# Optimization experiments

Hardware: AMD Instinct MI355X
Metric: run time of the kernel (lower is better)

The kernel has to match this reference:

```python
import jax, jax.numpy as jnp
import numpy as np

B, F_, E = 4096, 40, 64
T, M, H = 2, 3, 1
EPS = 1e-5


def setup_inputs() -> dict:
    key = jax.random.key(0)
    ks = jax.random.split(key, 8)
    def xavier(k, shape, fan_in, fan_out):
        a = float(np.sqrt(6.0 / (fan_in + fan_out)))
        return jax.random.uniform(k, shape, jnp.float32, -a, a)
    x = jax.random.normal(ks[0], (B, F_, E), jnp.float32)
    masker = xavier(ks[1], (T, M, F_, F_), F_, F_)
    ln_gamma = jnp.ones((F_,), jnp.float32)
    ln_beta = jnp.zeros((F_,), jnp.float32)
    w_t = xavier(ks[2], (1, T, H, 2 * E, E), 2 * E, E)
    b_t = xavier(ks[3], (T, H, F_, E), F_, E)
    nbn = T * F_ * 2 * E
    bn_gamma = jnp.ones((nbn,), jnp.float32)
    bn_beta = jnp.zeros((nbn,), jnp.float32)
    bn_mean = jnp.zeros((nbn,), jnp.float32)
    bn_var = jnp.ones((nbn,), jnp.float32)
    gate_w = xavier(ks[4], (F_ * E, F_), F_ * E, F_)
    gate_b = jnp.zeros((F_,), jnp.float32)
    return {"x": x, "masker": masker, "ln_gamma": ln_gamma, "ln_beta": ln_beta,
            "w_t": w_t, "b_t": b_t, "bn_gamma": bn_gamma, "bn_beta": bn_beta,
            "bn_mean": bn_mean, "bn_var": bn_var, "gate_w": gate_w, "gate_b": gate_b}


def reference(x, masker, ln_gamma, ln_beta, w_t, b_t, bn_gamma, bn_beta, bn_mean, bn_var, gate_w, gate_b):
    b = x.shape[0]
    # broadcast input across towers: (B, T, F, E)
    xt = jnp.broadcast_to(x[:, None], (b, T, F_, E))
    # masked adjacency construction (per tower)
    adj = jax.nn.relu(jnp.prod(masker, axis=1))            # (T, F, F)
    mask = (adj != 0).astype(x.dtype)
    # LayerNorm over dim -2 (applied to transposed adj in torch)
    t = jnp.swapaxes(adj, -1, -2)
    mu = t.mean(-1, keepdims=True)
    var = t.var(-1, keepdims=True)
    t = (t - mu) / jnp.sqrt(var + EPS) * ln_gamma + ln_beta
    adj = jnp.swapaxes(t, -1, -2)
    logits = adj + (1.0 - mask) * (-1e9) + jnp.eye(F_, dtype=x.dtype)
    adj = jax.nn.softmax(logits, axis=1) * mask            # softmax over source-field dim
    xcur = xt
    for idx in range(H):
        # neighbor aggregation: nei[b,t,f,e] = sum_g x[b,t,g,e] * adj[t,g,f]
        nei = jnp.einsum('btge,tgf->btfe', xcur, adj)
        xc = jnp.concatenate([xcur, nei], axis=-1)         # (B, T, F, 2E)
        flat = xc.reshape(b, -1)                           # BatchNorm1d, inference mode
        flat = (flat - bn_mean) / jnp.sqrt(bn_var + EPS) * bn_gamma + bn_beta
        xc = flat.reshape(b, T, F_, 2 * E)
        xcur = jnp.einsum('btfk,tke->btfe', xc, w_t[0, :, idx]) + b_t[:, idx]
    # gating over fields
    g = xcur.reshape(b, T, F_ * E) @ gate_w + gate_b       # (B, T, F)
    w = jax.nn.softmax(g, axis=2)
    return jnp.sum(xcur * w[..., None], axis=2)            # (B, T, E)
```

## Files before the change

### kernel.cpp

```cpp
#include <hip/hip_runtime.h>
#include <hip/hip_bf16.h>
#include <math.h>

#define Fdim 40
#define Edim 64
#define Tdim 2
#define EPSV 1e-5f

typedef __attribute__((ext_vector_type(8))) short short8;
typedef __attribute__((ext_vector_type(4))) float f32x4;

__device__ __forceinline__ short f2b(float f) {
    unsigned u = __builtin_bit_cast(unsigned, f);
    unsigned r = (u + 0x7fffu + ((u >> 16) & 1u)) >> 16;
    return (short)r;
}
__device__ __forceinline__ float b2f(short h) {
    unsigned u = ((unsigned)(unsigned short)h) << 16;
    return __builtin_bit_cast(float, u);
}
__device__ __forceinline__ f32x4 mfma16(short8 a, short8 b, f32x4 c) {
    return __builtin_amdgcn_mfma_f32_16x16x32_bf16(a, b, c, 0, 0, 0);
}
__device__ __forceinline__ int swz(int f, int e2 ) {
    return (f * 128 + e2) ^ ((f & 7) << 4);
}

#define BUFS 5152


__global__ void adj_kernel(const float* __restrict__ masker,
                           const float* __restrict__ ln_gamma,
                           const float* __restrict__ ln_beta,
                           short* __restrict__ adjF) {
    const int t = blockIdx.x;
    const int tid = threadIdx.x;
    __shared__ float araw[Fdim][Fdim];

    for (int i = tid; i < Fdim * Fdim; i += 64) {
        int g = i / Fdim, ff = i % Fdim;
        const float* mb = masker + t * (3 * Fdim * Fdim) + g * Fdim + ff;
        float p = mb[0] * mb[Fdim * Fdim] * mb[2 * Fdim * Fdim];
        araw[g][ff] = p > 0.f ? p : 0.f;
    }
    __syncthreads();

    const int f = tid;
    float vals[Fdim];
    if (f < 40) {
        float mu = 0.f, m2 = 0.f;
        #pragma unroll
        for (int g = 0; g < Fdim; ++g) {
            float v = araw[g][f];
            mu += v; m2 += v * v;
        }
        mu *= (1.f / Fdim); m2 *= (1.f / Fdim);
        float inv = rsqrtf(m2 - mu * mu + EPSV);

        float mx = -1e30f;
        #pragma unroll
        for (int g = 0; g < Fdim; ++g) {
            float v = araw[g][f];
            float l = (v - mu) * inv * ln_gamma[g] + ln_beta[g];
            if (v == 0.f) l += -1e9f;
            if (g == f) l += 1.f;
            vals[g] = l;
            mx = fmaxf(mx, l);
        }
        float den = 0.f;
        #pragma unroll
        for (int g = 0; g < Fdim; ++g) {
            float p = expf(vals[g] - mx);
            vals[g] = p;
            den += p;
        }
        float rden = 1.f / den;
        #pragma unroll
        for (int g = 0; g < Fdim; ++g) {
            float msk = (araw[g][f] != 0.f) ? 1.f : 0.f;
            vals[g] = vals[g] * rden * msk;
        }
    }
    if (f < 48) {
        int er = f & 15, mt = f >> 4;
        short8* dst = (short8*)adjF;
        #pragma unroll
        for (int kt = 0; kt < 2; ++kt) {
            #pragma unroll
            for (int qq = 0; qq < 4; ++qq) {
                short8 v;
                #pragma unroll
                for (int j = 0; j < 8; ++j) {
                    int g = kt * 32 + qq * 8 + j;
                    v[j] = (f < 40 && g < 40) ? f2b(vals[g]) : (short)0;
                }
                dst[((t * 3 + mt) * 2 + kt) * 64 + qq * 16 + er] = v;
            }
        }
    }
}

__global__ void prep_kernel(const float* __restrict__ w_t,
                            const float* __restrict__ gate_w,
                            const float* __restrict__ bn_gamma,
                            const float* __restrict__ bn_beta,
                            const float* __restrict__ bn_mean,
                            const float* __restrict__ bn_var,
                            const float* __restrict__ b_t,
                            short* __restrict__ WF,
                            short* __restrict__ gwF,
                            float* __restrict__ bnSxF,
                            float* __restrict__ bnOxF,
                            float* __restrict__ bn2SF,
                            float* __restrict__ bn2OF,
                            float* __restrict__ btF) {
    int i = blockIdx.x * 256 + threadIdx.x;
    if (i < 16384) {
        int j = i & 7, l = (i >> 3) & 63, nt = (i >> 9) & 3, kt = (i >> 11) & 3, t = i >> 13;
        int k = kt * 32 + (l >> 4) * 8 + j, e = nt * 16 + (l & 15);
        WF[i] = f2b(w_t[t * 8192 + k * 64 + e]);
    } else if (i < 139264) {
        int idx = i - 16384;
        int j = idx & 7, l = (idx >> 3) & 63, r = idx >> 9;
        int nt = r % 3, kk = r / 3;
        int fo = nt * 16 + (l & 15), k = kk * 32 + (l >> 4) * 8 + j;
        gwF[idx] = (fo < 40) ? f2b(gate_w[(size_t)k * 40 + fo]) : (short)0;
    } else if (i < 145408) {
        int idx = i - 139264;
        int c = idx & 3, l = (idx >> 2) & 63, h = (idx >> 8) & 1, kt = (idx >> 9) & 1, tm = idx >> 10;
        int mt = tm % 3, t = tm / 3;
        int f = mt * 16 + (l & 15), k = kt * 32 + (l >> 4) * 8 + h * 4 + c;
        float sv = 0.f, ov = 0.f;
        if (f < 40) {
            int src = t * 5120 + f * 128 + k;
            sv = bn_gamma[src] * rsqrtf(bn_var[src] + EPSV);
            ov = bn_beta[src] - bn_mean[src] * sv;
        }
        bnSxF[idx] = sv; bnOxF[idx] = ov;
    } else if (i < 151552) {
        int idx = i - 145408;
        int rr = idx & 3, l = (idx >> 2) & 63, nt = (idx >> 8) & 3, tm = idx >> 10;
        int mt = tm % 3, t = tm / 3;
        int f = mt * 16 + (l >> 4) * 4 + rr, e = nt * 16 + (l & 15);
        float sv = 0.f, ov = 0.f;
        if (f < 40) {
            int src = t * 5120 + f * 128 + 64 + e;
            sv = bn_gamma[src] * rsqrtf(bn_var[src] + EPSV);
            ov = bn_beta[src] - bn_mean[src] * sv;
        }
        bn2SF[idx] = sv; bn2OF[idx] = ov;
    } else if (i < 157696) {
        int idx = i - 151552;
        int rr = idx & 3, l = (idx >> 2) & 63, nt = (idx >> 8) & 3, tm = idx >> 10;
        int mt = tm % 3, t = tm / 3;
        int f = mt * 16 + (l >> 4) * 4 + rr, e = nt * 16 + (l & 15);
        btF[idx] = (f < 40) ? b_t[t * 2560 + f * 64 + e] : 0.f;
    }
}

__global__ __launch_bounds__(512, 4) void main_kernel(
    const float* __restrict__ x,
    const short* __restrict__ adjF,
    const short* __restrict__ WF,
    const short* __restrict__ gwF,
    const f32x4* __restrict__ bnSxF,
    const f32x4* __restrict__ bnOxF,
    const f32x4* __restrict__ bn2SF,
    const f32x4* __restrict__ bn2OF,
    const f32x4* __restrict__ btF,
    const float* __restrict__ gate_b,
    float* __restrict__ out)
{
    extern __shared__ char smem[];
    const int tid = threadIdx.x;
    const int w = tid >> 6, lane = tid & 63;
    const int er = lane & 15, q = lane >> 4;
    const int s = w >> 1, t = w & 1;
    const int bbase = blockIdx.x * 4;

    char* buf = smem + w * BUFS;
    f32x4* gred = (f32x4*)(smem + 8 * BUFS);
    float* g_lds = (float*)(smem + 8 * BUFS + 6144);

    const float* xb = x + (size_t)(bbase + s) * 2560;
    const short8* adjF8 = (const short8*)adjF;
    const short8* WF8   = (const short8*)WF;
    const short8* gwF8  = (const short8*)gwF;

    short8 Bf[2][4];
    #pragma unroll
    for (int nt = 0; nt < 4; ++nt) {
        const float* xe = xb + nt * 16 + er;
        short8 v0;
        #pragma unroll
        for (int j = 0; j < 8; ++j) v0[j] = f2b(xe[(q * 8 + j) * 64]);
        Bf[0][nt] = v0;
        short8 v1 = {0, 0, 0, 0, 0, 0, 0, 0};
        if (q == 0) {
            #pragma unroll
            for (int j = 0; j < 8; ++j) v1[j] = f2b(xe[(32 + j) * 64]);
        }
        Bf[1][nt] = v1;
    }

    #pragma unroll
    for (int mt = 0; mt < 3; ++mt) {
        short8 A0 = adjF8[((t * 3 + mt) * 2 + 0) * 64 + lane];
        short8 A1 = adjF8[((t * 3 + mt) * 2 + 1) * 64 + lane];
        #pragma unroll
        for (int nt = 0; nt < 4; ++nt) {
            f32x4 z = {0.f, 0.f, 0.f, 0.f};
            z = mfma16(A0, Bf[0][nt], z);
            f32x4 acc = mfma16(A1, Bf[1][nt], z);
            f32x4 s2 = bn2SF[((t * 3 + mt) * 4 + nt) * 64 + lane];
            f32x4 o2 = bn2OF[((t * 3 + mt) * 4 + nt) * 64 + lane];
            int e = nt * 16 + er;
            #pragma unroll
            for (int r = 0; r < 4; ++r) {
                int f = mt * 16 + q * 4 + r;
                if (f < 40) {
                    float vv = acc[r] * s2[r] + o2[r];
                    *(short*)(buf + swz(f, e * 2)) = f2b(vv);
                }
            }
        }
    }

    #pragma unroll
    for (int mt = 0; mt < 3; ++mt) {
        f32x4 acc[4];
        #pragma unroll
        for (int nt = 0; nt < 4; ++nt) { f32x4 z = {0.f,0.f,0.f,0.f}; acc[nt] = z; }
        #pragma unroll
        for (int kt = 0; kt < 4; ++kt) {
            short8 A;
            if (kt < 2) {
                int f = mt * 16 + er;
                if (f < 40) {
                    const float4* xp = (const float4*)(xb + f * 64 + kt * 32 + q * 8);
                    float4 x0 = xp[0], x1 = xp[1];
                    int fb = (((t * 3 + mt) * 2 + kt) * 2) * 64 + lane;
                    f32x4 s0 = bnSxF[fb], s1 = bnSxF[fb + 64];
                    f32x4 o0 = bnOxF[fb], o1 = bnOxF[fb + 64];
                    A[0] = f2b(x0.x * s0[0] + o0[0]);
                    A[1] = f2b(x0.y * s0[1] + o0[1]);
                    A[2] = f2b(x0.z * s0[2] + o0[2]);
                    A[3] = f2b(x0.w * s0[3] + o0[3]);
                    A[4] = f2b(x1.x * s1[0] + o1[0]);
                    A[5] = f2b(x1.y * s1[1] + o1[1]);
                    A[6] = f2b(x1.z * s1[2] + o1[2]);
                    A[7] = f2b(x1.w * s1[3] + o1[3]);
                } else {
                    short8 za = {0,0,0,0,0,0,0,0};
                    A = za;
                }
            } else {
                int f = mt * 16 + er;
                int fr = (f < 40) ? f : (f - 8);
                A = *(const short8*)(buf + swz(fr, (kt - 2) * 64 + q * 16));
            }
            #pragma unroll
            for (int nt = 0; nt < 4; ++nt) {
                short8 B = WF8[((t * 4 + kt) * 4 + nt) * 64 + lane];
                acc[nt] = mfma16(A, B, acc[nt]);
            }
        }
        #pragma unroll
        for (int nt = 0; nt < 4; ++nt) {
            f32x4 bt4 = btF[((t * 3 + mt) * 4 + nt) * 64 + lane];
            int e = nt * 16 + er;
            #pragma unroll
            for (int r = 0; r < 4; ++r) {
                int f = mt * 16 + q * 4 + r;
                if (f < 40) {
                    float vv = acc[nt][r] + bt4[r];
                    *(short*)(buf + swz(f, e * 2)) = f2b(vv);
                }
            }
        }
    }

    __syncthreads();

    f32x4 g0 = {0.f,0.f,0.f,0.f}, g1 = g0, g2 = g0;
    {
        const char* abase = smem + (er & 7) * BUFS;
        #pragma unroll
        for (int kk = 0; kk < 10; ++kk) {
            int step = w * 10 + kk;
            int k0 = step * 32;
            int f = k0 >> 6;
            short8 A = *(const short8*)(abase + swz(f, (k0 & 63) * 2 + q * 16));
            const short8* gp = gwF8 + (size_t)step * 3 * 64 + lane;
            g0 = mfma16(A, gp[0], g0);
            g1 = mfma16(A, gp[64], g1);
            g2 = mfma16(A, gp[128], g2);
        }
    }
    if (w < 4 && q < 2) {
        gred[(w * 3 + 0) * 32 + (lane & 31)] = g0;
        gred[(w * 3 + 1) * 32 + (lane & 31)] = g1;
        gred[(w * 3 + 2) * 32 + (lane & 31)] = g2;
    }
    __syncthreads();
    if (w >= 4 && q < 2) {
        gred[((w - 4) * 3 + 0) * 32 + (lane & 31)] += g0;
        gred[((w - 4) * 3 + 1) * 32 + (lane & 31)] += g1;
        gred[((w - 4) * 3 + 2) * 32 + (lane & 31)] += g2;
    }
    __syncthreads();

    if (tid < 192) {
        int nt = tid >> 6, l = tid & 63;
        if (l < 32) {
            int rer = l & 15, rq = l >> 4;
            f32x4 v = gred[(0 * 3 + nt) * 32 + l];
            #pragma unroll
            for (int ww = 1; ww < 4; ++ww) v += gred[(ww * 3 + nt) * 32 + l];
            int fo = nt * 16 + rer;
            if (fo < 40) {
                float gb = gate_b[fo];
                #pragma unroll
                for (int r = 0; r < 4; ++r)
                    g_lds[(rq * 4 + r) * 40 + fo] = v[r] + gb;
            }
        }
    }
    __syncthreads();

    {
        int st = tid >> 6, e = tid & 63;
        const float* gr = g_lds + st * 40;
        const char* bufr = smem + st * BUFS;
        float m = gr[0];
        #pragma unroll
        for (int f2 = 1; f2 < 40; ++f2) m = fmaxf(m, gr[f2]);
        float den = 0.f, o = 0.f;
        #pragma unroll
        for (int f2 = 0; f2 < 40; ++f2) {
            float p = __expf(gr[f2] - m);
            den += p;
            short xv = *(const short*)(bufr + swz(f2, e * 2));
            o += p * b2f(xv);
        }
        out[(size_t)(bbase * 2 + st) * 64 + e] = o / den;
    }
}

extern "C" void kernel_launch(void* const* d_in, const int* in_sizes, int n_in,
                              void* d_out, int out_size, void* d_ws, size_t ws_size,
                              hipStream_t stream) {
    (void)in_sizes; (void)n_in; (void)out_size; (void)ws_size;
    const float* x        = (const float*)d_in[0];
    const float* masker   = (const float*)d_in[1];
    const float* ln_gamma = (const float*)d_in[2];
    const float* ln_beta  = (const float*)d_in[3];
    const float* w_t      = (const float*)d_in[4];
    const float* b_t      = (const float*)d_in[5];
    const float* bn_gamma = (const float*)d_in[6];
    const float* bn_beta  = (const float*)d_in[7];
    const float* bn_mean  = (const float*)d_in[8];
    const float* bn_var   = (const float*)d_in[9];
    const float* gate_w   = (const float*)d_in[10];
    const float* gate_b   = (const float*)d_in[11];
    float* out = (float*)d_out;

    short* adjFp  = (short*)d_ws;
    short* WFp    = adjFp + 6144;
    short* gwFp   = WFp + 16384;
    float* bnSxFp = (float*)(gwFp + 122880);
    float* bnOxFp = bnSxFp + 6144;
    float* bn2SFp = bnOxFp + 6144;
    float* bn2OFp = bn2SFp + 6144;
    float* btFp   = bn2OFp + 6144;

    adj_kernel<<<Tdim, 64, 0, stream>>>(masker, ln_gamma, ln_beta, adjFp);
    prep_kernel<<<616, 256, 0, stream>>>(w_t, gate_w, bn_gamma, bn_beta, bn_mean,
                                         bn_var, b_t, WFp, gwFp, bnSxFp, bnOxFp,
                                         bn2SFp, bn2OFp, btFp);

    constexpr int SMEM_BYTES = 8 * BUFS + 4 * 3 * 32 * 16 + 8 * 40 * 4;
    main_kernel<<<1024, 512, SMEM_BYTES, stream>>>(
        x, adjFp, (const short*)WFp, (const short*)gwFp,
        (const f32x4*)bnSxFp, (const f32x4*)bnOxFp,
        (const f32x4*)bn2SFp, (const f32x4*)bn2OFp,
        (const f32x4*)btFp, gate_b, out);
}
```

Before: 73.76 us.

## Split main kernel into xcur and gate kernels via workspace, merge setup kernels

Merges the adjacency and weight-prep kernels into one launch to save a kernel launch. Splits the fused main kernel into an xcur kernel (256 threads, one wave per sample-tower) that writes bf16 intermediate results to a global workspace, and a gate kernel that reloads them and performs the gating GEMM and softmax. The aim is smaller blocks with better occupancy and less LDS per block. The cost is an extra global round trip of about 40MB of bf16 data plus one more launch, and the new path only runs when the workspace is large enough; otherwise it falls back to the original fused kernel.

```diff
diff --git a/kernel.cpp b/kernel.cpp
--- a/kernel.cpp
+++ b/kernel.cpp
@@ -29,92 +29,94 @@
 #define BUFS 5152
 
 
-__global__ void adj_kernel(const float* __restrict__ masker,
-                           const float* __restrict__ ln_gamma,
-                           const float* __restrict__ ln_beta,
-                           short* __restrict__ adjF) {
-    const int t = blockIdx.x;
+__global__ void setup_kernel(const float* __restrict__ masker,
+                             const float* __restrict__ ln_gamma,
+                             const float* __restrict__ ln_beta,
+                             const float* __restrict__ w_t,
+                             const float* __restrict__ gate_w,
+                             const float* __restrict__ bn_gamma,
+                             const float* __restrict__ bn_beta,
+                             const float* __restrict__ bn_mean,
+                             const float* __restrict__ bn_var,
+                             const float* __restrict__ b_t,
+                             short* __restrict__ adjF,
+                             short* __restrict__ WF,
+                             short* __restrict__ gwF,
+                             float* __restrict__ bnSxF,
+                             float* __restrict__ bnOxF,
+                             float* __restrict__ bn2SF,
+                             float* __restrict__ bn2OF,
+                             float* __restrict__ btF) {
+    const int bid = blockIdx.x;
     const int tid = threadIdx.x;
-    __shared__ float araw[Fdim][Fdim];
-
-    for (int i = tid; i < Fdim * Fdim; i += 64) {
-        int g = i / Fdim, ff = i % Fdim;
-        const float* mb = masker + t * (3 * Fdim * Fdim) + g * Fdim + ff;
-        float p = mb[0] * mb[Fdim * Fdim] * mb[2 * Fdim * Fdim];
-        araw[g][ff] = p > 0.f ? p : 0.f;
-    }
-    __syncthreads();
-
-    const int f = tid;
-    float vals[Fdim];
-    if (f < 40) {
-        float mu = 0.f, m2 = 0.f;
-        #pragma unroll
-        for (int g = 0; g < Fdim; ++g) {
-            float v = araw[g][f];
-            mu += v; m2 += v * v;
-        }
-        mu *= (1.f / Fdim); m2 *= (1.f / Fdim);
-        float inv = rsqrtf(m2 - mu * mu + EPSV);
-
-        float mx = -1e30f;
-        #pragma unroll
-        for (int g = 0; g < Fdim; ++g) {
-            float v = araw[g][f];
-            float l = (v - mu) * inv * ln_gamma[g] + ln_beta[g];
-            if (v == 0.f) l += -1e9f;
-            if (g == f) l += 1.f;
-            vals[g] = l;
-            mx = fmaxf(mx, l);
-        }
-        float den = 0.f;
-        #pragma unroll
-        for (int g = 0; g < Fdim; ++g) {
-            float p = expf(vals[g] - mx);
-            vals[g] = p;
-            den += p;
-        }
-        float rden = 1.f / den;
-        #pragma unroll
-        for (int g = 0; g < Fdim; ++g) {
-            float msk = (araw[g][f] != 0.f) ? 1.f : 0.f;
-            vals[g] = vals[g] * rden * msk;
-        }
-    }
-    if (f < 48) {
-        int er = f & 15, mt = f >> 4;
-        short8* dst = (short8*)adjF;
-        #pragma unroll
-        for (int kt = 0; kt < 2; ++kt) {
-            #pragma unroll
-            for (int qq = 0; qq < 4; ++qq) {
-                short8 v;
+
+    if (bid >= 616) {
+        const int t = bid - 616;
+        __shared__ float araw[Fdim][Fdim];
+        for (int i = tid; i < Fdim * Fdim; i += 256) {
+            int g = i / Fdim, ff = i % Fdim;
+            const float* mb = masker + t * (3 * Fdim * Fdim) + g * Fdim + ff;
+            float p = mb[0] * mb[Fdim * Fdim] * mb[2 * Fdim * Fdim];
+            araw[g][ff] = p > 0.f ? p : 0.f;
+        }
+        __syncthreads();
+
+        const int f = tid;
+        float vals[Fdim];
+        if (f < 40) {
+            float mu = 0.f, m2 = 0.f;
+            #pragma unroll
+            for (int g = 0; g < Fdim; ++g) {
+                float v = araw[g][f];
+                mu += v; m2 += v * v;
+            }
+            mu *= (1.f / Fdim); m2 *= (1.f / Fdim);
+            float inv = rsqrtf(m2 - mu * mu + EPSV);
+            float mx = -1e30f;
+            #pragma unroll
+            for (int g = 0; g < Fdim; ++g) {
+                float v = araw[g][f];
+                float l = (v - mu) * inv * ln_gamma[g] + ln_beta[g];
+                if (v == 0.f) l += -1e9f;
+                if (g == f) l += 1.f;
+                vals[g] = l;
+                mx = fmaxf(mx, l);
+            }
+            float den = 0.f;
+            #pragma unroll
+            for (int g = 0; g < Fdim; ++g) {
+                float p = expf(vals[g] - mx);
+                vals[g] = p;
+                den += p;
+            }
+            float rden = 1.f / den;
+            #pragma unroll
+            for (int g = 0; g < Fdim; ++g) {
+                float msk = (araw[g][f] != 0.f) ? 1.f : 0.f;
+                vals[g] = vals[g] * rden * msk;
+            }
+        }
+        if (f < 48) {
+            int er = f & 15, mt = f >> 4;
+            short8* dst = (short8*)adjF;
+            #pragma unroll
+            for (int kt = 0; kt < 2; ++kt) {
                 #pragma unroll
-                for (int j = 0; j < 8; ++j) {
-                    int g = kt * 32 + qq * 8 + j;
-                    v[j] = (f < 40 && g < 40) ? f2b(vals[g]) : (short)0;
+                for (int qq = 0; qq < 4; ++qq) {
+                    short8 v;
+                    #pragma unroll
+                    for (int j = 0; j < 8; ++j) {
+                        int g = kt * 32 + qq * 8 + j;
+                        v[j] = (f < 40 && g < 40) ? f2b(vals[g]) : (short)0;
+                    }
+                    dst[((t * 3 + mt) * 2 + kt) * 64 + qq * 16 + er] = v;
                 }
-                dst[((t * 3 + mt) * 2 + kt) * 64 + qq * 16 + er] = v;
-            }
-        }
-    }
-}
-
-__global__ void prep_kernel(const float* __restrict__ w_t,
-                            const float* __restrict__ gate_w,
-                            const float* __restrict__ bn_gamma,
-                            const float* __restrict__ bn_beta,
-                            const float* __restrict__ bn_mean,
-                            const float* __restrict__ bn_var,
-                            const float* __restrict__ b_t,
-                            short* __restrict__ WF,
-                            short* __restrict__ gwF,
-                            float* __restrict__ bnSxF,
-                            float* __restrict__ bnOxF,
-                            float* __restrict__ bn2SF,
-                            float* __restrict__ bn2OF,
-                            float* __restrict__ btF) {
-    int i = blockIdx.x * 256 + threadIdx.x;
+            }
+        }
+        return;
+    }
+
+    int i = bid * 256 + tid;
     if (i < 16384) {
         int j = i & 7, l = (i >> 3) & 63, nt = (i >> 9) & 3, kt = (i >> 11) & 3, t = i >> 13;
         int k = kt * 32 + (l >> 4) * 8 + j, e = nt * 16 + (l & 15);
@@ -158,34 +160,28 @@
     }
 }
 
-__global__ __launch_bounds__(512, 4) void main_kernel(
+__global__ __launch_bounds__(256, 4) void xcur_kernel(
     const float* __restrict__ x,
     const short* __restrict__ adjF,
     const short* __restrict__ WF,
-    const short* __restrict__ gwF,
     const f32x4* __restrict__ bnSxF,
     const f32x4* __restrict__ bnOxF,
     const f32x4* __restrict__ bn2SF,
     const f32x4* __restrict__ bn2OF,
     const f32x4* __restrict__ btF,
-    const float* __restrict__ gate_b,
-    float* __restrict__ out)
+    short* __restrict__ xws)
 {
-    extern __shared__ char smem[];
+    __shared__ char smem[4 * BUFS];
     const int tid = threadIdx.x;
     const int w = tid >> 6, lane = tid & 63;
     const int er = lane & 15, q = lane >> 4;
-    const int s = w >> 1, t = w & 1;
-    const int bbase = blockIdx.x * 4;
+    const int st = blockIdx.x * 4 + w;
+    const int s = st >> 1, t = st & 1;
 
     char* buf = smem + w * BUFS;
-    f32x4* gred = (f32x4*)(smem + 8 * BUFS);
-    float* g_lds = (float*)(smem + 8 * BUFS + 6144);
-
-    const float* xb = x + (size_t)(bbase + s) * 2560;
+    const float* xb = x + (size_t)s * 2560;
     const short8* adjF8 = (const short8*)adjF;
     const short8* WF8   = (const short8*)WF;
-    const short8* gwF8  = (const short8*)gwF;
 
     short8 Bf[2][4];
     #pragma unroll
@@ -280,6 +276,231 @@
         }
     }
 
+    {
+        short8* dst = (short8*)(xws + (size_t)st * 2560);
+        const short8* src = (const short8*)buf;
+        #pragma unroll
+        for (int i = 0; i < 5; ++i) dst[i * 64 + lane] = src[i * 64 + lane];
+    }
+}
+
+__global__ __launch_bounds__(256, 4) void gate_kernel(
+    const short* __restrict__ xws,
+    const short* __restrict__ gwF,
+    const float* __restrict__ gate_b,
+    float* __restrict__ out)
+{
+    extern __shared__ char smem[];
+    const int tid = threadIdx.x;
+    const int w = tid >> 6, lane = tid & 63;
+    const int er = lane & 15, q = lane >> 4;
+    const int stbase = blockIdx.x * 8;
+
+    f32x4* gred = (f32x4*)(smem + 8 * BUFS);
+    float* g_lds = (float*)(smem + 8 * BUFS + 3072);
+    const short8* gwF8 = (const short8*)gwF;
+
+    {
+        const short8* gsrc = (const short8*)(xws + (size_t)stbase * 2560);
+        #pragma unroll
+        for (int i = 0; i < 10; ++i) {
+            int c = i * 256 + tid;
+            int stl = c / 320, off = c - stl * 320;
+            short8 v = gsrc[c];
+            *(short8*)(smem + stl * BUFS + off * 16) = v;
+        }
+    }
+    __syncthreads();
+
+    f32x4 g0 = {0.f,0.f,0.f,0.f}, g1 = g0, g2 = g0;
+    {
+        const char* abase = smem + (er & 7) * BUFS;
+        #pragma unroll
+        for (int kk = 0; kk < 20; ++kk) {
+            int step = w * 20 + kk;
+            int k0 = step * 32;
+            int f = k0 >> 6;
+            short8 A = *(const short8*)(abase + swz(f, (k0 & 63) * 2 + q * 16));
+            const short8* gp = gwF8 + (size_t)step * 3 * 64 + lane;
+            g0 = mfma16(A, gp[0], g0);
+            g1 = mfma16(A, gp[64], g1);
+            g2 = mfma16(A, gp[128], g2);
+        }
+    }
+    if (w < 2 && q < 2) {
+        gred[(w * 3 + 0) * 32 + (lane & 31)] = g0;
+        gred[(w * 3 + 1) * 32 + (lane & 31)] = g1;
+        gred[(w * 3 + 2) * 32 + (lane & 31)] = g2;
+    }
+    __syncthreads();
+    if (w >= 2 && q < 2) {
+        gred[((w - 2) * 3 + 0) * 32 + (lane & 31)] += g0;
+        gred[((w - 2) * 3 + 1) * 32 + (lane & 31)] += g1;
+        gred[((w - 2) * 3 + 2) * 32 + (lane & 31)] += g2;
+    }
+    __syncthreads();
+
+    if (tid < 192) {
+        int nt = tid >> 6, l = tid & 63;
+        if (l < 32) {
+            int rer = l & 15, rq = l >> 4;
+            f32x4 v = gred[(0 * 3 + nt) * 32 + l] + gred[(1 * 3 + nt) * 32 + l];
+            int fo = nt * 16 + rer;
+            if (fo < 40) {
+                float gb = gate_b[fo];
+                #pragma unroll
+                for (int r = 0; r < 4; ++r)
+                    g_lds[(rq * 4 + r) * 40 + fo] = v[r] + gb;
+            }
+        }
+    }
+    __syncthreads();
+
+    {
+        int e = tid & 63;
+        #pragma unroll
+        for (int rep = 0; rep < 2; ++rep) {
+            int st = (tid >> 6) + rep * 4;
+            const float* gr = g_lds + st * 40;
+            const char* bufr = smem + st * BUFS;
+            float m = gr[0];
+            #pragma unroll
+            for (int f2 = 1; f2 < 40; ++f2) m = fmaxf(m, gr[f2]);
+            float den = 0.f, o = 0.f;
+            #pragma unroll
+            for (int f2 = 0; f2 < 40; ++f2) {
+                float p = __expf(gr[f2] - m);
+                den += p;
+                short xv = *(const short*)(bufr + swz(f2, e * 2));
+                o += p * b2f(xv);
+            }
+            out[(size_t)(stbase + st) * 64 + e] = o / den;
+        }
+    }
+}
+
+__global__ __launch_bounds__(512, 4) void main_fallback(
+    const float* __restrict__ x,
+    const short* __restrict__ adjF,
+    const short* __restrict__ WF,
+    const short* __restrict__ gwF,
+    const f32x4* __restrict__ bnSxF,
+    const f32x4* __restrict__ bnOxF,
+    const f32x4* __restrict__ bn2SF,
+    const f32x4* __restrict__ bn2OF,
+    const f32x4* __restrict__ btF,
+    const float* __restrict__ gate_b,
+    float* __restrict__ out)
+{
+    extern __shared__ char smem[];
+    const int tid = threadIdx.x;
+    const int w = tid >> 6, lane = tid & 63;
+    const int er = lane & 15, q = lane >> 4;
+    const int s = w >> 1, t = w & 1;
+    const int bbase = blockIdx.x * 4;
+
+    char* buf = smem + w * BUFS;
+    f32x4* gred = (f32x4*)(smem + 8 * BUFS);
+    float* g_lds = (float*)(smem + 8 * BUFS + 6144);
+
+    const float* xb = x + (size_t)(bbase + s) * 2560;
+    const short8* adjF8 = (const short8*)adjF;
+    const short8* WF8   = (const short8*)WF;
+    const short8* gwF8  = (const short8*)gwF;
+
+    short8 Bf[2][4];
+    #pragma unroll
+    for (int nt = 0; nt < 4; ++nt) {
+        const float* xe = xb + nt * 16 + er;
+        short8 v0;
+        #pragma unroll
+        for (int j = 0; j < 8; ++j) v0[j] = f2b(xe[(q * 8 + j) * 64]);
+        Bf[0][nt] = v0;
+        short8 v1 = {0, 0, 0, 0, 0, 0, 0, 0};
+        if (q == 0) {
+            #pragma unroll
+            for (int j = 0; j < 8; ++j) v1[j] = f2b(xe[(32 + j) * 64]);
+        }
+        Bf[1][nt] = v1;
+    }
+
+    #pragma unroll
+    for (int mt = 0; mt < 3; ++mt) {
+        short8 A0 = adjF8[((t * 3 + mt) * 2 + 0) * 64 + lane];
+        short8 A1 = adjF8[((t * 3 + mt) * 2 + 1) * 64 + lane];
+        #pragma unroll
+        for (int nt = 0; nt < 4; ++nt) {
+            f32x4 z = {0.f, 0.f, 0.f, 0.f};
+            z = mfma16(A0, Bf[0][nt], z);
+            f32x4 acc = mfma16(A1, Bf[1][nt], z);
+            f32x4 s2 = bn2SF[((t * 3 + mt) * 4 + nt) * 64 + lane];
+            f32x4 o2 = bn2OF[((t * 3 + mt) * 4 + nt) * 64 + lane];
+            int e = nt * 16 + er;
+            #pragma unroll
+            for (int r = 0; r < 4; ++r) {
+                int f = mt * 16 + q * 4 + r;
+                if (f < 40) {
+                    float vv = acc[r] * s2[r] + o2[r];
+                    *(short*)(buf + swz(f, e * 2)) = f2b(vv);
+                }
+            }
+        }
+    }
+
+    #pragma unroll
+    for (int mt = 0; mt < 3; ++mt) {
+        f32x4 acc[4];
+        #pragma unroll
+        for (int nt = 0; nt < 4; ++nt) { f32x4 z = {0.f,0.f,0.f,0.f}; acc[nt] = z; }
+        #pragma unroll
+        for (int kt = 0; kt < 4; ++kt) {
+            short8 A;
+            if (kt < 2) {
+                int f = mt * 16 + er;
+                if (f < 40) {
+                    const float4* xp = (const float4*)(xb + f * 64 + kt * 32 + q * 8);
+                    float4 x0 = xp[0], x1 = xp[1];
+                    int fb = (((t * 3 + mt) * 2 + kt) * 2) * 64 + lane;
+                    f32x4 s0 = bnSxF[fb], s1 = bnSxF[fb + 64];
+                    f32x4 o0 = bnOxF[fb], o1 = bnOxF[fb + 64];
+                    A[0] = f2b(x0.x * s0[0] + o0[0]);
+                    A[1] = f2b(x0.y * s0[1] + o0[1]);
+                    A[2] = f2b(x0.z * s0[2] + o0[2]);
+                    A[3] = f2b(x0.w * s0[3] + o0[3]);
+                    A[4] = f2b(x1.x * s1[0] + o1[0]);
+                    A[5] = f2b(x1.y * s1[1] + o1[1]);
+                    A[6] = f2b(x1.z * s1[2] + o1[2]);
+                    A[7] = f2b(x1.w * s1[3] + o1[3]);
+                } else {
+                    short8 za = {0,0,0,0,0,0,0,0};
+                    A = za;
+                }
+            } else {
+                int f = mt * 16 + er;
+                int fr = (f < 40) ? f : (f - 8);
+                A = *(const short8*)(buf + swz(fr, (kt - 2) * 64 + q * 16));
+            }
+            #pragma unroll
+            for (int nt = 0; nt < 4; ++nt) {
+                short8 B = WF8[((t * 4 + kt) * 4 + nt) * 64 + lane];
+                acc[nt] = mfma16(A, B, acc[nt]);
+            }
+        }
+        #pragma unroll
+        for (int nt = 0; nt < 4; ++nt) {
+            f32x4 bt4 = btF[((t * 3 + mt) * 4 + nt) * 64 + lane];
+            int e = nt * 16 + er;
+            #pragma unroll
+            for (int r = 0; r < 4; ++r) {
+                int f = mt * 16 + q * 4 + r;
+                if (f < 40) {
+                    float vv = acc[nt][r] + bt4[r];
+                    *(short*)(buf + swz(f, e * 2)) = f2b(vv);
+                }
+            }
+        }
+    }
+
     __syncthreads();
 
     f32x4 g0 = {0.f,0.f,0.f,0.f}, g1 = g0, g2 = g0;
@@ -350,7 +571,7 @@
 extern "C" void kernel_launch(void* const* d_in, const int* in_sizes, int n_in,
                               void* d_out, int out_size, void* d_ws, size_t ws_size,
                               hipStream_t stream) {
-    (void)in_sizes; (void)n_in; (void)out_size; (void)ws_size;
+    (void)in_sizes; (void)n_in; (void)out_size;
     const float* x        = (const float*)d_in[0];
     const float* masker   = (const float*)d_in[1];
     const float* ln_gamma = (const float*)d_in[2];
@@ -373,16 +594,29 @@
     float* bn2SFp = bnOxFp + 6144;
     float* bn2OFp = bn2SFp + 6144;
     float* btFp   = bn2OFp + 6144;
-
-    adj_kernel<<<Tdim, 64, 0, stream>>>(masker, ln_gamma, ln_beta, adjFp);
-    prep_kernel<<<616, 256, 0, stream>>>(w_t, gate_w, bn_gamma, bn_beta, bn_mean,
-                                         bn_var, b_t, WFp, gwFp, bnSxFp, bnOxFp,
-                                         bn2SFp, bn2OFp, btFp);
-
-    constexpr int SMEM_BYTES = 8 * BUFS + 4 * 3 * 32 * 16 + 8 * 40 * 4;
-    main_kernel<<<1024, 512, SMEM_BYTES, stream>>>(
-        x, adjFp, (const short*)WFp, (const short*)gwFp,
-        (const f32x4*)bnSxFp, (const f32x4*)bnOxFp,
-        (const f32x4*)bn2SFp, (const f32x4*)bn2OFp,
-        (const f32x4*)btFp, gate_b, out);
-}
+    short* xws    = (short*)((char*)d_ws + 413696);
+
+    setup_kernel<<<618, 256, 0, stream>>>(masker, ln_gamma, ln_beta, w_t, gate_w,
+                                          bn_gamma, bn_beta, bn_mean, bn_var, b_t,
+                                          adjFp, WFp, gwFp, bnSxFp, bnOxFp,
+                                          bn2SFp, bn2OFp, btFp);
+
+    const size_t need = 413696 + (size_t)8192 * 5120;
+    if (ws_size >= need) {
+        xcur_kernel<<<2048, 256, 0, stream>>>(
+            x, adjFp, (const short*)WFp,
+            (const f32x4*)bnSxFp, (const f32x4*)bnOxFp,
+            (const f32x4*)bn2SFp, (const f32x4*)bn2OFp,
+            (const f32x4*)btFp, xws);
+        constexpr int SMEM2 = 8 * BUFS + 3072 + 1280;
+        gate_kernel<<<1024, 256, SMEM2, stream>>>(xws, (const short*)gwFp,
+                                                  gate_b, out);
+    } else {
+        constexpr int SMEM_FB = 8 * BUFS + 4 * 3 * 32 * 16 + 8 * 40 * 4;
+        main_fallback<<<1024, 512, SMEM_FB, stream>>>(
+            x, adjFp, (const short*)WFp, (const short*)gwFp,
+            (const f32x4*)bnSxFp, (const f32x4*)bnOxFp,
+            (const f32x4*)bn2SFp, (const f32x4*)bn2OFp,
+            (const f32x4*)btFp, gate_b, out);
+    }
+}
```

After: 88.81 us. +20.4%, slower.

## Stage x tile in LDS as bf16 with coalesced loads; merge setup kernels

Applied to the files above, without the earlier changes.

The main kernel now loads the four-sample x tile with coalesced float4 reads, converts it to bf16 once, and stores it in a swizzled LDS staging area. The B-fragment gathers and the BN-scaled A-fragment loads then read from LDS instead of doing strided global loads. The adj and prep kernels are merged into one setup launch to save a kernel launch. The launch-bounds occupancy hint drops from 4 to 2 blocks per CU, and the extra LDS lowers possible occupancy. The gate reduction buffers are aliased onto the x staging region.

```diff
diff --git a/kernel.cpp b/kernel.cpp
--- a/kernel.cpp
+++ b/kernel.cpp
@@ -25,96 +25,102 @@
 __device__ __forceinline__ int swz(int f, int e2 ) {
     return (f * 128 + e2) ^ ((f & 7) << 4);
 }
+__device__ __forceinline__ int swx(int b) {
+    return b ^ (((b >> 7) & 7) << 4);
+}
 
 #define BUFS 5152
-
-
-__global__ void adj_kernel(const float* __restrict__ masker,
-                           const float* __restrict__ ln_gamma,
-                           const float* __restrict__ ln_beta,
-                           short* __restrict__ adjF) {
-    const int t = blockIdx.x;
+#define XSTG 20480
+
+
+__global__ void setup_kernel(const float* __restrict__ masker,
+                             const float* __restrict__ ln_gamma,
+                             const float* __restrict__ ln_beta,
+                             const float* __restrict__ w_t,
+                             const float* __restrict__ gate_w,
+                             const float* __restrict__ bn_gamma,
+                             const float* __restrict__ bn_beta,
+                             const float* __restrict__ bn_mean,
+                             const float* __restrict__ bn_var,
+                             const float* __restrict__ b_t,
+                             short* __restrict__ adjF,
+                             short* __restrict__ WF,
+                             short* __restrict__ gwF,
+                             float* __restrict__ bnSxF,
+                             float* __restrict__ bnOxF,
+                             float* __restrict__ bn2SF,
+                             float* __restrict__ bn2OF,
+                             float* __restrict__ btF) {
+    const int bid = blockIdx.x;
     const int tid = threadIdx.x;
-    __shared__ float araw[Fdim][Fdim];
-
-    for (int i = tid; i < Fdim * Fdim; i += 64) {
-        int g = i / Fdim, ff = i % Fdim;
-        const float* mb = masker + t * (3 * Fdim * Fdim) + g * Fdim + ff;
-        float p = mb[0] * mb[Fdim * Fdim] * mb[2 * Fdim * Fdim];
-        araw[g][ff] = p > 0.f ? p : 0.f;
-    }
-    __syncthreads();
-
-    const int f = tid;
-    float vals[Fdim];
-    if (f < 40) {
-        float mu = 0.f, m2 = 0.f;
-        #pragma unroll
-        for (int g = 0; g < Fdim; ++g) {
-            float v = araw[g][f];
-            mu += v; m2 += v * v;
-        }
-        mu *= (1.f / Fdim); m2 *= (1.f / Fdim);
-        float inv = rsqrtf(m2 - mu * mu + EPSV);
-
-        float mx = -1e30f;
-        #pragma unroll
-        for (int g = 0; g < Fdim; ++g) {
-            float v = araw[g][f];
-            float l = (v - mu) * inv * ln_gamma[g] + ln_beta[g];
-            if (v == 0.f) l += -1e9f;
-            if (g == f) l += 1.f;
-            vals[g] = l;
-            mx = fmaxf(mx, l);
-        }
-        float den = 0.f;
-        #pragma unroll
-        for (int g = 0; g < Fdim; ++g) {
-            float p = expf(vals[g] - mx);
-            vals[g] = p;
-            den += p;
-        }
-        float rden = 1.f / den;
-        #pragma unroll
-        for (int g = 0; g < Fdim; ++g) {
-            float msk = (araw[g][f] != 0.f) ? 1.f : 0.f;
-            vals[g] = vals[g] * rden * msk;
-        }
-    }
-    if (f < 48) {
-        int er = f & 15, mt = f >> 4;
-        short8* dst = (short8*)adjF;
-        #pragma unroll
-        for (int kt = 0; kt < 2; ++kt) {
-            #pragma unroll
-            for (int qq = 0; qq < 4; ++qq) {
-                short8 v;
+
+    if (bid >= 616) {
+        const int t = bid - 616;
+        __shared__ float araw[Fdim][Fdim];
+        for (int i = tid; i < Fdim * Fdim; i += 256) {
+            int g = i / Fdim, ff = i % Fdim;
+            const float* mb = masker + t * (3 * Fdim * Fdim) + g * Fdim + ff;
+            float p = mb[0] * mb[Fdim * Fdim] * mb[2 * Fdim * Fdim];
+            araw[g][ff] = p > 0.f ? p : 0.f;
+        }
+        __syncthreads();
+
+        const int f = tid;
+        float vals[Fdim];
+        if (f < 40) {
+            float mu = 0.f, m2 = 0.f;
+            #pragma unroll
+            for (int g = 0; g < Fdim; ++g) {
+                float v = araw[g][f];
+                mu += v; m2 += v * v;
+            }
+            mu *= (1.f / Fdim); m2 *= (1.f / Fdim);
+            float inv = rsqrtf(m2 - mu * mu + EPSV);
+            float mx = -1e30f;
+            #pragma unroll
+            for (int g = 0; g < Fdim; ++g) {
+                float v = araw[g][f];
+                float l = (v - mu) * inv * ln_gamma[g] + ln_beta[g];
+                if (v == 0.f) l += -1e9f;
+                if (g == f) l += 1.f;
+                vals[g] = l;
+                mx = fmaxf(mx, l);
+            }
+            float den = 0.f;
+            #pragma unroll
+            for (int g = 0; g < Fdim; ++g) {
+                float p = expf(vals[g] - mx);
+                vals[g] = p;
+                den += p;
+            }
+            float rden = 1.f / den;
+            #pragma unroll
+            for (int g = 0; g < Fdim; ++g) {
+                float msk = (araw[g][f] != 0.f) ? 1.f : 0.f;
+                vals[g] = vals[g] * rden * msk;
+            }
+        }
+        if (f < 48) {
+            int er = f & 15, mt = f >> 4;
+            short8* dst = (short8*)adjF;
+            #pragma unroll
+            for (int kt = 0; kt < 2; ++kt) {
                 #pragma unroll
-                for (int j = 0; j < 8; ++j) {
-                    int g = kt * 32 + qq * 8 + j;
-                    v[j] = (f < 40 && g < 40) ? f2b(vals[g]) : (short)0;
+                for (int qq = 0; qq < 4; ++qq) {
+                    short8 v;
+                    #pragma unroll
+                    for (int j = 0; j < 8; ++j) {
+                        int g = kt * 32 + qq * 8 + j;
+                        v[j] = (f < 40 && g < 40) ? f2b(vals[g]) : (short)0;
+                    }
+                    dst[((t * 3 + mt) * 2 + kt) * 64 + qq * 16 + er] = v;
                 }
-                dst[((t * 3 + mt) * 2 + kt) * 64 + qq * 16 + er] = v;
-            }
-        }
-    }
-}
-
-__global__ void prep_kernel(const float* __restrict__ w_t,
-                            const float* __restrict__ gate_w,
-                            const float* __restrict__ bn_gamma,
-                            const float* __restrict__ bn_beta,
-                            const float* __restrict__ bn_mean,
-                            const float* __restrict__ bn_var,
-                            const float* __restrict__ b_t,
-                            short* __restrict__ WF,
-                            short* __restrict__ gwF,
-                            float* __restrict__ bnSxF,
-                            float* __restrict__ bnOxF,
-                            float* __restrict__ bn2SF,
-                            float* __restrict__ bn2OF,
-                            float* __restrict__ btF) {
-    int i = blockIdx.x * 256 + threadIdx.x;
+            }
+        }
+        return;
+    }
+
+    int i = bid * 256 + tid;
     if (i < 16384) {
         int j = i & 7, l = (i >> 3) & 63, nt = (i >> 9) & 3, kt = (i >> 11) & 3, t = i >> 13;
         int k = kt * 32 + (l >> 4) * 8 + j, e = nt * 16 + (l & 15);
@@ -158,7 +164,7 @@
     }
 }
 
-__global__ __launch_bounds__(512, 4) void main_kernel(
+__global__ __launch_bounds__(512, 2) void main_kernel(
     const float* __restrict__ x,
     const short* __restrict__ adjF,
     const short* __restrict__ WF,
@@ -178,27 +184,47 @@
     const int s = w >> 1, t = w & 1;
     const int bbase = blockIdx.x * 4;
 
-    char* buf = smem + w * BUFS;
-    f32x4* gred = (f32x4*)(smem + 8 * BUFS);
-    float* g_lds = (float*)(smem + 8 * BUFS + 6144);
-
-    const float* xb = x + (size_t)(bbase + s) * 2560;
+    char* buf = smem + XSTG + w * BUFS;
+    f32x4* gred = (f32x4*)smem;
+    float* g_lds = (float*)(smem + 6144);
+    const char* xs = smem + s * 5120;
+
     const short8* adjF8 = (const short8*)adjF;
     const short8* WF8   = (const short8*)WF;
     const short8* gwF8  = (const short8*)gwF;
 
+    {
+        const float4* xall = (const float4*)(x + (size_t)bbase * 2560);
+        #pragma unroll
+        for (int i = 0; i < 3; ++i) {
+            int c = tid + i * 512;
+            if (c < 1280) {
+                int ss = c / 320, cc = c - ss * 320;
+                float4 a = xall[ss * 640 + cc * 2];
+                float4 b = xall[ss * 640 + cc * 2 + 1];
+                short8 v;
+                v[0] = f2b(a.x); v[1] = f2b(a.y); v[2] = f2b(a.z); v[3] = f2b(a.w);
+                v[4] = f2b(b.x); v[5] = f2b(b.y); v[6] = f2b(b.z); v[7] = f2b(b.w);
+                *(short8*)(smem + ss * 5120 + swx(cc * 16)) = v;
+            }
+        }
+    }
+    __syncthreads();
+
     short8 Bf[2][4];
     #pragma unroll
     for (int nt = 0; nt < 4; ++nt) {
-        const float* xe = xb + nt * 16 + er;
+        int e2 = (nt * 16 + er) * 2;
         short8 v0;
         #pragma unroll
-        for (int j = 0; j < 8; ++j) v0[j] = f2b(xe[(q * 8 + j) * 64]);
+        for (int j = 0; j < 8; ++j)
+            v0[j] = *(const short*)(xs + (((q * 8 + j) * 128 + e2) ^ (j << 4)));
         Bf[0][nt] = v0;
         short8 v1 = {0, 0, 0, 0, 0, 0, 0, 0};
         if (q == 0) {
             #pragma unroll
-            for (int j = 0; j < 8; ++j) v1[j] = f2b(xe[(32 + j) * 64]);
+            for (int j = 0; j < 8; ++j)
+                v1[j] = *(const short*)(xs + (((32 + j) * 128 + e2) ^ (j << 4)));
         }
         Bf[1][nt] = v1;
     }
@@ -237,19 +263,18 @@
             if (kt < 2) {
                 int f = mt * 16 + er;
                 if (f < 40) {
-                    const float4* xp = (const float4*)(xb + f * 64 + kt * 32 + q * 8);
-                    float4 x0 = xp[0], x1 = xp[1];
+                    short8 xv = *(const short8*)(xs + swx(f * 128 + kt * 64 + q * 16));
                     int fb = (((t * 3 + mt) * 2 + kt) * 2) * 64 + lane;
                     f32x4 s0 = bnSxF[fb], s1 = bnSxF[fb + 64];
                     f32x4 o0 = bnOxF[fb], o1 = bnOxF[fb + 64];
-                    A[0] = f2b(x0.x * s0[0] + o0[0]);
-                    A[1] = f2b(x0.y * s0[1] + o0[1]);
-                    A[2] = f2b(x0.z * s0[2] + o0[2]);
-                    A[3] = f2b(x0.w * s0[3] + o0[3]);
-                    A[4] = f2b(x1.x * s1[0] + o1[0]);
-                    A[5] = f2b(x1.y * s1[1] + o1[1]);
-                    A[6] = f2b(x1.z * s1[2] + o1[2]);
-                    A[7] = f2b(x1.w * s1[3] + o1[3]);
+                    A[0] = f2b(b2f(xv[0]) * s0[0] + o0[0]);
+                    A[1] = f2b(b2f(xv[1]) * s0[1] + o0[1]);
+                    A[2] = f2b(b2f(xv[2]) * s0[2] + o0[2]);
+                    A[3] = f2b(b2f(xv[3]) * s0[3] + o0[3]);
+                    A[4] = f2b(b2f(xv[4]) * s1[0] + o1[0]);
+                    A[5] = f2b(b2f(xv[5]) * s1[1] + o1[1]);
+                    A[6] = f2b(b2f(xv[6]) * s1[2] + o1[2]);
+                    A[7] = f2b(b2f(xv[7]) * s1[3] + o1[3]);
                 } else {
                     short8 za = {0,0,0,0,0,0,0,0};
                     A = za;
@@ -284,7 +309,7 @@
 
     f32x4 g0 = {0.f,0.f,0.f,0.f}, g1 = g0, g2 = g0;
     {
-        const char* abase = smem + (er & 7) * BUFS;
+        const char* abase = smem + XSTG + (er & 7) * BUFS;
         #pragma unroll
         for (int kk = 0; kk < 10; ++kk) {
             int step = w * 10 + kk;
@@ -331,7 +356,7 @@
     {
         int st = tid >> 6, e = tid & 63;
         const float* gr = g_lds + st * 40;
-        const char* bufr = smem + st * BUFS;
+        const char* bufr = smem + XSTG + st * BUFS;
         float m = gr[0];
         #pragma unroll
         for (int f2 = 1; f2 < 40; ++f2) m = fmaxf(m, gr[f2]);
@@ -374,12 +399,12 @@
     float* bn2OFp = bn2SFp + 6144;
     float* btFp   = bn2OFp + 6144;
 
-    adj_kernel<<<Tdim, 64, 0, stream>>>(masker, ln_gamma, ln_beta, adjFp);
-    prep_kernel<<<616, 256, 0, stream>>>(w_t, gate_w, bn_gamma, bn_beta, bn_mean,
-                                         bn_var, b_t, WFp, gwFp, bnSxFp, bnOxFp,
-                                         bn2SFp, bn2OFp, btFp);
-
-    constexpr int SMEM_BYTES = 8 * BUFS + 4 * 3 * 32 * 16 + 8 * 40 * 4;
+    setup_kernel<<<618, 256, 0, stream>>>(masker, ln_gamma, ln_beta, w_t, gate_w,
+                                          bn_gamma, bn_beta, bn_mean, bn_var, b_t,
+                                          adjFp, WFp, gwFp, bnSxFp, bnOxFp,
+                                          bn2SFp, bn2OFp, btFp);
+
+    constexpr int SMEM_BYTES = XSTG + 8 * BUFS;
     main_kernel<<<1024, 512, SMEM_BYTES, stream>>>(
         x, adjFp, (const short*)WFp, (const short*)gwFp,
         (const f32x4*)bnSxFp, (const f32x4*)bnOxFp,
```

New measurement: 82.29 us. +11.6%, slower.
